# Kernel tuning notes

Measured on AMD Instinct MI355X. Metric: run time of the kernel, lower is better.

The kernel has to match this reference:

```python
import jax, jax.numpy as jnp
import numpy as np

NUM_HEADS = 16
HEAD_DIM = 128  # embed_dim 2048 / 16 heads


def setup_inputs() -> dict:
    key = jax.random.key(0)
    x = jax.random.normal(key, (2, 2048, 2048), dtype=jnp.float32)
    return {"x": x}


def reference(x):
    # EvoAttn forward: V-only causal self-attention (q = k = v = reshaped x).
    B, L, E = x.shape
    H, D = NUM_HEADS, HEAD_DIM
    v = x.reshape(B, L, H, D).transpose(0, 2, 1, 3)  # (B, H, L, D)
    scale = 1.0 / jnp.sqrt(jnp.asarray(D, dtype=x.dtype))
    scores = jnp.einsum("bhqd,bhkd->bhqk", v, v) * scale  # (B, H, L, L)
    causal = jnp.tril(jnp.ones((L, L), dtype=bool))
    scores = jnp.where(causal[None, None], scores, jnp.asarray(-jnp.inf, dtype=scores.dtype))
    p = jax.nn.softmax(scores, axis=-1)
    y = jnp.einsum("bhqk,bhkd->bhqd", p, v)  # (B, H, L, D)
    return y.transpose(0, 2, 1, 3).reshape(B, L, E)
```

## Files before the change

### kernel.cpp

```cpp
#include <hip/hip_runtime.h>


#define TL 2048
#define TE 2048
#define TD 128
#define QB 64
#define KB 64
#define NT 32
#define TILE_B 16384
#define KV_REGION (2 * 16 * NT * TILE_B)
#define WS_NEED (2u * (unsigned)KV_REGION)

typedef __attribute__((ext_vector_type(8))) short bf16x8;
typedef __attribute__((ext_vector_type(4))) float f32x4;
typedef __attribute__((ext_vector_type(8))) unsigned short u16x8;
typedef __attribute__((ext_vector_type(4))) unsigned short u16x4;

#define SCALE_LOG2E 0.12751879f

__device__ __forceinline__ unsigned short f2bf(float f) {
  unsigned int u = __builtin_bit_cast(unsigned int, f);
  u += 0x7fffu + ((u >> 16) & 1u);
  return (unsigned short)(u >> 16);
}

__device__ __forceinline__ f32x4 mfma16(bf16x8 a, bf16x8 b, f32x4 c) {
  return __builtin_amdgcn_mfma_f32_16x16x32_bf16(a, b, c, 0, 0, 0);
}

__device__ __forceinline__ void gl_lds16(const void* g, void* l) {
  __builtin_amdgcn_global_load_lds(
      (__attribute__((address_space(1))) void*)(g),
      (__attribute__((address_space(3))) void*)(l), 16, 0, 0);
}

__device__ __forceinline__ void stage_tile(const float* __restrict__ src,
                                           unsigned short* kv, unsigned short* kvt,
                                           int t) {
  const int kr = (t >> 4) << 2;
  const int d0 = (t & 15) << 3;
  unsigned short c[4][8];
#pragma unroll
  for (int rr = 0; rr < 4; ++rr) {
    const float* p = src + (kr + rr) * TE + d0;
    const float4 a = *(const float4*)p;
    const float4 b = *(const float4*)(p + 4);
    c[rr][0] = f2bf(a.x); c[rr][1] = f2bf(a.y); c[rr][2] = f2bf(a.z); c[rr][3] = f2bf(a.w);
    c[rr][4] = f2bf(b.x); c[rr][5] = f2bf(b.y); c[rr][6] = f2bf(b.z); c[rr][7] = f2bf(b.w);
  }
#pragma unroll
  for (int rr = 0; rr < 4; ++rr) {
    const int r = kr + rr;
    u16x8 o = {c[rr][0], c[rr][1], c[rr][2], c[rr][3],
               c[rr][4], c[rr][5], c[rr][6], c[rr][7]};
    const int off = (r * 256 + d0 * 2) ^ ((r & 7) << 4);
    *(u16x8*)((char*)kv + off) = o;
  }
#pragma unroll
  for (int cc = 0; cc < 8; ++cc) {
    const int d = d0 + cc;
    u16x4 o = {c[0][cc], c[1][cc], c[2][cc], c[3][cc]};
    const int off = (d * 128 + kr * 2) ^ ((d & 7) << 4);
    *(u16x4*)((char*)kvt + off) = o;
  }
}

__device__ __forceinline__ bf16x8 ld256(const unsigned short* base, int row, int inrow) {
  const int off = (row * 256 + inrow) ^ ((row & 7) << 4);
  return *(const bf16x8*)((const char*)base + off);
}
__device__ __forceinline__ bf16x8 ld128(const unsigned short* base, int row, int inrow) {
  const int off = (row * 128 + inrow) ^ ((row & 7) << 4);
  return *(const bf16x8*)((const char*)base + off);
}

__global__ void __launch_bounds__(256)
prepack(const float* __restrict__ x, char* __restrict__ wsb) {
  __shared__ unsigned short kv[QB * TD];
  __shared__ unsigned short kvt[TD * KB];
  const int bid = blockIdx.x;
  const int kt = bid & 31;
  const int bh = bid >> 5;
  const int b = bh >> 4;
  const int h = bh & 15;
  const float* src = x + (size_t)b * TL * TE + h * TD + (size_t)kt * KB * TE;
  stage_tile(src, kv, kvt, threadIdx.x);
  __syncthreads();
  char* gkv = wsb + (size_t)bid * TILE_B;
  char* gkt = wsb + KV_REGION + (size_t)bid * TILE_B;
  const char* lv = (const char*)kv;
  const char* lt = (const char*)kvt;
  const int t = threadIdx.x;
#pragma unroll
  for (int i = 0; i < 4; ++i) {
    *(u16x8*)(gkv + t * 64 + i * 16) = *(const u16x8*)(lv + t * 64 + i * 16);
    *(u16x8*)(gkt + t * 64 + i * 16) = *(const u16x8*)(lt + t * 64 + i * 16);
  }
}

__global__ void __launch_bounds__(256)
evo_attn2(const char* __restrict__ wsb, float* __restrict__ out) {
  __shared__ char smem[3 * TILE_B + 8192];

  const int t = threadIdx.x;
  const int lane = t & 63;
  const int w = t >> 6;
  const int g = lane >> 4;
  const int q15 = lane & 15;

  const int bh = blockIdx.x & 31;
  const int qt = 31 - (blockIdx.x >> 5);
  const int b = bh >> 4;
  const int h = bh & 15;
  const int q0 = qt * QB;

  const char* gkv = wsb + (size_t)bh * (NT * TILE_B);
  const char* gkt = wsb + KV_REGION + (size_t)bh * (NT * TILE_B);

  unsigned short* kvt = (unsigned short*)(smem + 2 * TILE_B);
  unsigned short* plw = (unsigned short*)(smem + 3 * TILE_B) + w * (16 * KB);

#define STAGE_KV(BUFI, KT)                                                 \
  {                                                                        \
    char* dst_ = smem + (BUFI) * TILE_B;                                   \
    const char* src_ = gkv + (KT) * TILE_B;                                \
    _Pragma("unroll")                                                      \
    for (int i_ = 0; i_ < 4; ++i_) {                                       \
      const int c_ = (w * 4 + i_) * 1024;                                  \
      gl_lds16(src_ + c_ + lane * 16, dst_ + c_);                          \
    }                                                                      \
  }
#define STAGE_KT(KT)                                                       \
  {                                                                        \
    char* dst_ = smem + 2 * TILE_B;                                        \
    const char* src_ = gkt + (KT) * TILE_B;                                \
    _Pragma("unroll")                                                      \
    for (int i_ = 0; i_ < 4; ++i_) {                                       \
      const int c_ = (w * 4 + i_) * 1024;                                  \
      gl_lds16(src_ + c_ + lane * 16, dst_ + c_);                          \
    }                                                                      \
  }

  STAGE_KV(0, qt);
  STAGE_KT(qt);
  asm volatile("s_waitcnt vmcnt(0)" ::: "memory");
  __builtin_amdgcn_s_barrier();
  asm volatile("" ::: "memory");

  bf16x8 qf[4];
#pragma unroll
  for (int c = 0; c < 4; ++c)
    qf[c] = ld256((const unsigned short*)smem, 16 * w + q15, c * 64 + g * 16);

  f32x4 acc[8];
#pragma unroll
  for (int dt = 0; dt < 8; ++dt) acc[dt] = (f32x4){0.f, 0.f, 0.f, 0.f};
  float mrun = -1e30f;
  float lrun = 0.f;

  for (int s = 0; s <= qt; ++s) {
    if (s < qt) STAGE_KV((s + 1) & 1, s);

    if (s > 0) {
      if (s < qt) asm volatile("s_waitcnt vmcnt(8)" ::: "memory");
      else        asm volatile("s_waitcnt vmcnt(4)" ::: "memory");
      __builtin_amdgcn_s_barrier();
      asm volatile("" ::: "memory");
    }
    const unsigned short* kv = (const unsigned short*)(smem + (s & 1) * TILE_B);

    float sv[16];
    __builtin_amdgcn_s_setprio(1);
#pragma unroll
    for (int kt2 = 0; kt2 < 4; ++kt2) {
      f32x4 st = (f32x4){0.f, 0.f, 0.f, 0.f};
#pragma unroll
      for (int c = 0; c < 4; ++c) {
        bf16x8 kf = ld256(kv, kt2 * 16 + q15, c * 64 + g * 16);
        st = mfma16(kf, qf[c], st);
      }
#pragma unroll
      for (int r = 0; r < 4; ++r) sv[kt2 * 4 + r] = st[r] * SCALE_LOG2E;
    }
    __builtin_amdgcn_s_setprio(0);

    if (s == 0) {
      const int qrel = 16 * w + q15;
#pragma unroll
      for (int kt2 = 0; kt2 < 4; ++kt2)
#pragma unroll
        for (int r = 0; r < 4; ++r)
          if (kt2 * 16 + g * 4 + r > qrel) sv[kt2 * 4 + r] = -1e30f;
    }

    float tmax = sv[0];
#pragma unroll
    for (int i = 1; i < 16; ++i) tmax = fmaxf(tmax, sv[i]);
    tmax = fmaxf(tmax, __shfl_xor(tmax, 16));
    tmax = fmaxf(tmax, __shfl_xor(tmax, 32));

    const float mnew = fmaxf(mrun, tmax);
    const float al = exp2f(mrun - mnew);
    mrun = mnew;

    float psum = 0.f;
    unsigned short pb[16];
#pragma unroll
    for (int i = 0; i < 16; ++i) {
      const float p = exp2f(sv[i] - mnew);
      psum += p;
      pb[i] = f2bf(p);
    }
    lrun = lrun * al + psum;

#pragma unroll
    for (int kt2 = 0; kt2 < 4; ++kt2) {
      u16x4 o = {pb[kt2 * 4], pb[kt2 * 4 + 1], pb[kt2 * 4 + 2], pb[kt2 * 4 + 3]};
      const int off = (q15 * 128 + kt2 * 32 + g * 8) ^ ((q15 & 7) << 4);
      *(u16x4*)((char*)plw + off) = o;
    }
    asm volatile("s_waitcnt lgkmcnt(0)" ::: "memory");

    if (s > 0) {
      if (s < qt) asm volatile("s_waitcnt vmcnt(4)" ::: "memory");
      else        asm volatile("s_waitcnt vmcnt(0)" ::: "memory");
      __builtin_amdgcn_s_barrier();
      asm volatile("" ::: "memory");
    }

    float ar[4];
#pragma unroll
    for (int r = 0; r < 4; ++r) ar[r] = __shfl(al, g * 4 + r);
#pragma unroll
    for (int dt = 0; dt < 8; ++dt)
#pragma unroll
      for (int r = 0; r < 4; ++r) acc[dt][r] *= ar[r];

    bf16x8 pa0 = ld128(plw, q15, g * 16);
    bf16x8 pa1 = ld128(plw, q15, 64 + g * 16);
    __builtin_amdgcn_s_setprio(1);
#pragma unroll
    for (int dt = 0; dt < 8; ++dt) {
      bf16x8 vb0 = ld128(kvt, dt * 16 + q15, g * 16);
      bf16x8 vb1 = ld128(kvt, dt * 16 + q15, 64 + g * 16);
      acc[dt] = mfma16(pa0, vb0, acc[dt]);
      acc[dt] = mfma16(pa1, vb1, acc[dt]);
    }
    __builtin_amdgcn_s_setprio(0);

    if (s < qt) {
      __builtin_amdgcn_s_barrier();
      asm volatile("" ::: "memory");
      STAGE_KT(s);
    }
  }

  lrun += __shfl_xor(lrun, 16);
  lrun += __shfl_xor(lrun, 32);

  const float inv = 1.f / lrun;
  float ir[4];
#pragma unroll
  for (int r = 0; r < 4; ++r) ir[r] = __shfl(inv, g * 4 + r);

  float* ob = out + ((size_t)b * TL + q0 + 16 * w) * TE + h * TD;
#pragma unroll
  for (int dt = 0; dt < 8; ++dt)
#pragma unroll
    for (int r = 0; r < 4; ++r)
      ob[(g * 4 + r) * TE + dt * 16 + q15] = acc[dt][r] * ir[r];
}

__global__ void __launch_bounds__(256)
evo_attn(const float* __restrict__ x, float* __restrict__ out) {
  __shared__ unsigned short kv[QB * TD];
  __shared__ unsigned short kvt[TD * KB];
  __shared__ unsigned short pl[4 * 16 * KB];

  const int t = threadIdx.x;
  const int lane = t & 63;
  const int w = t >> 6;
  const int g = lane >> 4;
  const int q15 = lane & 15;

  const int bh = blockIdx.x & 31;
  const int qt = 31 - (blockIdx.x >> 5);
  const int b = bh >> 4;
  const int h = bh & 15;
  const float* xb = x + (size_t)b * TL * TE + h * TD;
  const int q0 = qt * QB;

  stage_tile(xb + (size_t)q0 * TE, kv, kvt, t);
  __syncthreads();

  bf16x8 qf[4];
#pragma unroll
  for (int c = 0; c < 4; ++c)
    qf[c] = ld256(kv, 16 * w + q15, c * 64 + g * 16);

  f32x4 acc[8];
#pragma unroll
  for (int dt = 0; dt < 8; ++dt) acc[dt] = (f32x4){0.f, 0.f, 0.f, 0.f};
  float mrun = -1e30f;
  float lrun = 0.f;
  unsigned short* plw = pl + w * (16 * KB);

  for (int s = 0; s <= qt; ++s) {
    if (s > 0) {
      __syncthreads();
      stage_tile(xb + (size_t)(s - 1) * KB * TE, kv, kvt, t);
      __syncthreads();
    }
    float sv[16];
#pragma unroll
    for (int kt2 = 0; kt2 < 4; ++kt2) {
      f32x4 st = (f32x4){0.f, 0.f, 0.f, 0.f};
#pragma unroll
      for (int c = 0; c < 4; ++c) {
        bf16x8 kf = ld256(kv, kt2 * 16 + q15, c * 64 + g * 16);
        st = mfma16(kf, qf[c], st);
      }
#pragma unroll
      for (int r = 0; r < 4; ++r) sv[kt2 * 4 + r] = st[r] * SCALE_LOG2E;
    }
    if (s == 0) {
      const int qrel = 16 * w + q15;
#pragma unroll
      for (int kt2 = 0; kt2 < 4; ++kt2)
#pragma unroll
        for (int r = 0; r < 4; ++r)
          if (kt2 * 16 + g * 4 + r > qrel) sv[kt2 * 4 + r] = -1e30f;
    }
    float tmax = sv[0];
#pragma unroll
    for (int i = 1; i < 16; ++i) tmax = fmaxf(tmax, sv[i]);
    tmax = fmaxf(tmax, __shfl_xor(tmax, 16));
    tmax = fmaxf(tmax, __shfl_xor(tmax, 32));
    const float mnew = fmaxf(mrun, tmax);
    const float al = exp2f(mrun - mnew);
    mrun = mnew;
    float psum = 0.f;
    unsigned short pb[16];
#pragma unroll
    for (int i = 0; i < 16; ++i) {
      const float p = exp2f(sv[i] - mnew);
      psum += p;
      pb[i] = f2bf(p);
    }
    lrun = lrun * al + psum;
#pragma unroll
    for (int kt2 = 0; kt2 < 4; ++kt2) {
      u16x4 o = {pb[kt2 * 4], pb[kt2 * 4 + 1], pb[kt2 * 4 + 2], pb[kt2 * 4 + 3]};
      const int off = (q15 * 128 + kt2 * 32 + g * 8) ^ ((q15 & 7) << 4);
      *(u16x4*)((char*)plw + off) = o;
    }
    asm volatile("s_waitcnt lgkmcnt(0)" ::: "memory");
    float ar[4];
#pragma unroll
    for (int r = 0; r < 4; ++r) ar[r] = __shfl(al, g * 4 + r);
#pragma unroll
    for (int dt = 0; dt < 8; ++dt)
#pragma unroll
      for (int r = 0; r < 4; ++r) acc[dt][r] *= ar[r];
    bf16x8 pa0 = ld128(plw, q15, g * 16);
    bf16x8 pa1 = ld128(plw, q15, 64 + g * 16);
#pragma unroll
    for (int dt = 0; dt < 8; ++dt) {
      bf16x8 vb0 = ld128(kvt, dt * 16 + q15, g * 16);
      bf16x8 vb1 = ld128(kvt, dt * 16 + q15, 64 + g * 16);
      acc[dt] = mfma16(pa0, vb0, acc[dt]);
      acc[dt] = mfma16(pa1, vb1, acc[dt]);
    }
  }

  lrun += __shfl_xor(lrun, 16);
  lrun += __shfl_xor(lrun, 32);
  const float inv = 1.f / lrun;
  float ir[4];
#pragma unroll
  for (int r = 0; r < 4; ++r) ir[r] = __shfl(inv, g * 4 + r);
  float* ob = out + ((size_t)b * TL + q0 + 16 * w) * TE + h * TD;
#pragma unroll
  for (int dt = 0; dt < 8; ++dt)
#pragma unroll
    for (int r = 0; r < 4; ++r)
      ob[(g * 4 + r) * TE + dt * 16 + q15] = acc[dt][r] * ir[r];
}

extern "C" void kernel_launch(void* const* d_in, const int* in_sizes, int n_in,
                              void* d_out, int out_size, void* d_ws, size_t ws_size,
                              hipStream_t stream) {
  const float* x = (const float*)d_in[0];
  float* out = (float*)d_out;
  (void)in_sizes; (void)n_in; (void)out_size;
  if (ws_size >= (size_t)WS_NEED) {
    char* wsb = (char*)d_ws;
    prepack<<<dim3(1024), dim3(256), 0, stream>>>(x, wsb);
    evo_attn2<<<dim3(1024), dim3(256), 0, stream>>>(wsb, out);
  } else {
    evo_attn<<<dim3(1024), dim3(256), 0, stream>>>(x, out);
  }
}
```

Baseline: 99.80 us.

## Use 128-row query tiles with 8 waves sharing K/V staging per block

The main attention kernel now runs 512-thread blocks, each owning 128 query rows split across 8 waves, so every staged K/V tile feeds twice as many queries and global/LDS staging per query halves. Query tiles are issued in an interleaved long/short order to balance the causal workload across CUs. The online softmax folds the scale into an FMA and skips the accumulator rescale when no wave's max grows. The trade-offs are more barriers with idle waves on the diagonal step, a larger LDS footprint, and fewer blocks in flight.

Result: slower. 211.6 us (+112.0%).

```diff
diff --git a/kernel.cpp b/kernel.cpp
--- a/kernel.cpp
+++ b/kernel.cpp
@@ -1,14 +1,14 @@
 #include <hip/hip_runtime.h>
+#include <hip/hip_bf16.h>
 
 
 #define TL 2048
 #define TE 2048
 #define TD 128
-#define QB 64
 #define KB 64
-#define NT 32
+#define NTILES 32
 #define TILE_B 16384
-#define KV_REGION (2 * 16 * NT * TILE_B)
+#define KV_REGION (32 * NTILES * TILE_B)
 #define WS_NEED (2u * (unsigned)KV_REGION)
 
 typedef __attribute__((ext_vector_type(8))) short bf16x8;
@@ -19,9 +19,8 @@
 #define SCALE_LOG2E 0.12751879f
 
 __device__ __forceinline__ unsigned short f2bf(float f) {
-  unsigned int u = __builtin_bit_cast(unsigned int, f);
-  u += 0x7fffu + ((u >> 16) & 1u);
-  return (unsigned short)(u >> 16);
+  __hip_bfloat16 h = __float2bfloat16(f);
+  return __builtin_bit_cast(unsigned short, h);
 }
 
 __device__ __forceinline__ f32x4 mfma16(bf16x8 a, bf16x8 b, f32x4 c) {
@@ -76,7 +75,7 @@
 
 __global__ void __launch_bounds__(256)
 prepack(const float* __restrict__ x, char* __restrict__ wsb) {
-  __shared__ unsigned short kv[QB * TD];
+  __shared__ unsigned short kv[KB * TD];
   __shared__ unsigned short kvt[TD * KB];
   const int bid = blockIdx.x;
   const int kt = bid & 31;
@@ -98,9 +97,9 @@
   }
 }
 
-__global__ void __launch_bounds__(256)
+__global__ void __launch_bounds__(512, 4)
 evo_attn2(const char* __restrict__ wsb, float* __restrict__ out) {
-  __shared__ char smem[3 * TILE_B + 8192];
+  __shared__ char smem[4 * TILE_B];
 
   const int t = threadIdx.x;
   const int lane = t & 63;
@@ -109,48 +108,43 @@
   const int q15 = lane & 15;
 
   const int bh = blockIdx.x & 31;
-  const int qt = 31 - (blockIdx.x >> 5);
+  const int r_ = blockIdx.x >> 5;
+  const int QSEQ[16] = {15, 0, 13, 2, 11, 4, 9, 6, 8, 7, 10, 5, 12, 3, 14, 1};
+  const int q2 = QSEQ[r_];
   const int b = bh >> 4;
   const int h = bh & 15;
-  const int q0 = qt * QB;
-
-  const char* gkv = wsb + (size_t)bh * (NT * TILE_B);
-  const char* gkt = wsb + KV_REGION + (size_t)bh * (NT * TILE_B);
+  const int q0 = q2 * 128;
+  const int nt = 2 * q2 + 2;
+
+  const char* gkv = wsb + (size_t)bh * (NTILES * TILE_B);
+  const char* gkt = wsb + KV_REGION + (size_t)bh * (NTILES * TILE_B);
 
   unsigned short* kvt = (unsigned short*)(smem + 2 * TILE_B);
   unsigned short* plw = (unsigned short*)(smem + 3 * TILE_B) + w * (16 * KB);
 
-#define STAGE_KV(BUFI, KT)                                                 \
+#define STAGE(DSTOFF, SRCBASE, KT)                                         \
   {                                                                        \
-    char* dst_ = smem + (BUFI) * TILE_B;                                   \
-    const char* src_ = gkv + (KT) * TILE_B;                                \
+    char* dst_ = smem + (DSTOFF);                                          \
+    const char* src_ = (SRCBASE) + (size_t)(KT) * TILE_B;                  \
     _Pragma("unroll")                                                      \
-    for (int i_ = 0; i_ < 4; ++i_) {                                       \
-      const int c_ = (w * 4 + i_) * 1024;                                  \
+    for (int i_ = 0; i_ < 2; ++i_) {                                       \
+      const int c_ = (i_ * 8 + w) * 1024;                                  \
       gl_lds16(src_ + c_ + lane * 16, dst_ + c_);                          \
     }                                                                      \
   }
-#define STAGE_KT(KT)                                                       \
-  {                                                                        \
-    char* dst_ = smem + 2 * TILE_B;                                        \
-    const char* src_ = gkt + (KT) * TILE_B;                                \
-    _Pragma("unroll")                                                      \
-    for (int i_ = 0; i_ < 4; ++i_) {                                       \
-      const int c_ = (w * 4 + i_) * 1024;                                  \
-      gl_lds16(src_ + c_ + lane * 16, dst_ + c_);                          \
-    }                                                                      \
-  }
-
-  STAGE_KV(0, qt);
-  STAGE_KT(qt);
+
+  STAGE(0, gkv, 2 * q2);
+  STAGE(TILE_B, gkv, 2 * q2 + 1);
+  STAGE(2 * TILE_B, gkt, 2 * q2);
   asm volatile("s_waitcnt vmcnt(0)" ::: "memory");
   __builtin_amdgcn_s_barrier();
   asm volatile("" ::: "memory");
 
+  const unsigned short* qbuf = (const unsigned short*)(smem + ((w >= 4) ? TILE_B : 0));
   bf16x8 qf[4];
 #pragma unroll
   for (int c = 0; c < 4; ++c)
-    qf[c] = ld256((const unsigned short*)smem, 16 * w + q15, c * 64 + g * 16);
+    qf[c] = ld256(qbuf, (16 * w + q15) & 63, c * 64 + g * 16);
 
   f32x4 acc[8];
 #pragma unroll
@@ -158,101 +152,112 @@
   float mrun = -1e30f;
   float lrun = 0.f;
 
-  for (int s = 0; s <= qt; ++s) {
-    if (s < qt) STAGE_KV((s + 1) & 1, s);
-
+  for (int s = 0; s < nt; ++s) {
     if (s > 0) {
-      if (s < qt) asm volatile("s_waitcnt vmcnt(8)" ::: "memory");
-      else        asm volatile("s_waitcnt vmcnt(4)" ::: "memory");
+      if (s + 1 < nt) asm volatile("s_waitcnt vmcnt(4)" ::: "memory");
+      else            asm volatile("s_waitcnt vmcnt(2)" ::: "memory");
       __builtin_amdgcn_s_barrier();
       asm volatile("" ::: "memory");
     }
     const unsigned short* kv = (const unsigned short*)(smem + (s & 1) * TILE_B);
-
-    float sv[16];
-    __builtin_amdgcn_s_setprio(1);
-#pragma unroll
-    for (int kt2 = 0; kt2 < 4; ++kt2) {
-      f32x4 st = (f32x4){0.f, 0.f, 0.f, 0.f};
-#pragma unroll
-      for (int c = 0; c < 4; ++c) {
-        bf16x8 kf = ld256(kv, kt2 * 16 + q15, c * 64 + g * 16);
-        st = mfma16(kf, qf[c], st);
-      }
-#pragma unroll
-      for (int r = 0; r < 4; ++r) sv[kt2 * 4 + r] = st[r] * SCALE_LOG2E;
-    }
-    __builtin_amdgcn_s_setprio(0);
-
-    if (s == 0) {
-      const int qrel = 16 * w + q15;
-#pragma unroll
-      for (int kt2 = 0; kt2 < 4; ++kt2)
-#pragma unroll
-        for (int r = 0; r < 4; ++r)
-          if (kt2 * 16 + g * 4 + r > qrel) sv[kt2 * 4 + r] = -1e30f;
-    }
-
-    float tmax = sv[0];
-#pragma unroll
-    for (int i = 1; i < 16; ++i) tmax = fmaxf(tmax, sv[i]);
-    tmax = fmaxf(tmax, __shfl_xor(tmax, 16));
-    tmax = fmaxf(tmax, __shfl_xor(tmax, 32));
-
-    const float mnew = fmaxf(mrun, tmax);
-    const float al = exp2f(mrun - mnew);
-    mrun = mnew;
-
-    float psum = 0.f;
-    unsigned short pb[16];
-#pragma unroll
-    for (int i = 0; i < 16; ++i) {
-      const float p = exp2f(sv[i] - mnew);
-      psum += p;
-      pb[i] = f2bf(p);
-    }
-    lrun = lrun * al + psum;
-
-#pragma unroll
-    for (int kt2 = 0; kt2 < 4; ++kt2) {
-      u16x4 o = {pb[kt2 * 4], pb[kt2 * 4 + 1], pb[kt2 * 4 + 2], pb[kt2 * 4 + 3]};
-      const int off = (q15 * 128 + kt2 * 32 + g * 8) ^ ((q15 & 7) << 4);
-      *(u16x4*)((char*)plw + off) = o;
-    }
-    asm volatile("s_waitcnt lgkmcnt(0)" ::: "memory");
+    const bool inactive = (s == 1) && (w < 4);
+
+    float pf[16];
+    if (!inactive) {
+      float sv[16];
+      __builtin_amdgcn_s_setprio(1);
+#pragma unroll
+      for (int kt2 = 0; kt2 < 4; ++kt2) {
+        f32x4 st = (f32x4){0.f, 0.f, 0.f, 0.f};
+#pragma unroll
+        for (int c = 0; c < 4; ++c) {
+          bf16x8 kf = ld256(kv, kt2 * 16 + q15, c * 64 + g * 16);
+          st = mfma16(kf, qf[c], st);
+        }
+#pragma unroll
+        for (int r = 0; r < 4; ++r) sv[kt2 * 4 + r] = st[r];
+      }
+      __builtin_amdgcn_s_setprio(0);
+
+      if (s < 2 && ((s == 0) == (w < 4))) {
+        const int qrel = (16 * w + q15) & 63;
+#pragma unroll
+        for (int kt2 = 0; kt2 < 4; ++kt2)
+#pragma unroll
+          for (int r = 0; r < 4; ++r)
+            if (kt2 * 16 + g * 4 + r > qrel) sv[kt2 * 4 + r] = -1e30f;
+      }
+
+      float m0 = fmaxf(fmaxf(sv[0], sv[1]), fmaxf(sv[2], sv[3]));
+      float m1 = fmaxf(fmaxf(sv[4], sv[5]), fmaxf(sv[6], sv[7]));
+      float m2 = fmaxf(fmaxf(sv[8], sv[9]), fmaxf(sv[10], sv[11]));
+      float m3 = fmaxf(fmaxf(sv[12], sv[13]), fmaxf(sv[14], sv[15]));
+      float tmax = fmaxf(fmaxf(m0, m1), fmaxf(m2, m3));
+      tmax = fmaxf(tmax, __shfl_xor(tmax, 16));
+      tmax = fmaxf(tmax, __shfl_xor(tmax, 32));
+
+      if (__all(tmax <= mrun)) {
+        const float nmc = -mrun * SCALE_LOG2E;
+#pragma unroll
+        for (int i = 0; i < 16; ++i) pf[i] = exp2f(fmaf(sv[i], SCALE_LOG2E, nmc));
+      } else {
+        const float mnew = fmaxf(mrun, tmax);
+        const float al = exp2f((mrun - mnew) * SCALE_LOG2E);
+        mrun = mnew;
+        const float nmc = -mnew * SCALE_LOG2E;
+#pragma unroll
+        for (int i = 0; i < 16; ++i) pf[i] = exp2f(fmaf(sv[i], SCALE_LOG2E, nmc));
+        lrun *= al;
+        float ar[4];
+#pragma unroll
+        for (int r = 0; r < 4; ++r) ar[r] = __shfl(al, g * 4 + r);
+#pragma unroll
+        for (int dt = 0; dt < 8; ++dt)
+#pragma unroll
+          for (int r = 0; r < 4; ++r) acc[dt][r] *= ar[r];
+      }
+
+      float s01 = (pf[0] + pf[1]) + (pf[2] + pf[3]);
+      float s23 = (pf[4] + pf[5]) + (pf[6] + pf[7]);
+      float s45 = (pf[8] + pf[9]) + (pf[10] + pf[11]);
+      float s67 = (pf[12] + pf[13]) + (pf[14] + pf[15]);
+      lrun += (s01 + s23) + (s45 + s67);
+
+#pragma unroll
+      for (int kt2 = 0; kt2 < 4; ++kt2) {
+        u16x4 o = {f2bf(pf[kt2 * 4]), f2bf(pf[kt2 * 4 + 1]),
+                   f2bf(pf[kt2 * 4 + 2]), f2bf(pf[kt2 * 4 + 3])};
+        const int off = (q15 * 128 + kt2 * 32 + g * 8) ^ ((q15 & 7) << 4);
+        *(u16x4*)((char*)plw + off) = o;
+      }
+      asm volatile("s_waitcnt lgkmcnt(0)" ::: "memory");
+    }
 
     if (s > 0) {
-      if (s < qt) asm volatile("s_waitcnt vmcnt(4)" ::: "memory");
-      else        asm volatile("s_waitcnt vmcnt(0)" ::: "memory");
+      if (s + 1 < nt) asm volatile("s_waitcnt vmcnt(2)" ::: "memory");
+      else            asm volatile("s_waitcnt vmcnt(0)" ::: "memory");
       __builtin_amdgcn_s_barrier();
       asm volatile("" ::: "memory");
     }
 
-    float ar[4];
-#pragma unroll
-    for (int r = 0; r < 4; ++r) ar[r] = __shfl(al, g * 4 + r);
-#pragma unroll
-    for (int dt = 0; dt < 8; ++dt)
-#pragma unroll
-      for (int r = 0; r < 4; ++r) acc[dt][r] *= ar[r];
-
-    bf16x8 pa0 = ld128(plw, q15, g * 16);
-    bf16x8 pa1 = ld128(plw, q15, 64 + g * 16);
-    __builtin_amdgcn_s_setprio(1);
-#pragma unroll
-    for (int dt = 0; dt < 8; ++dt) {
-      bf16x8 vb0 = ld128(kvt, dt * 16 + q15, g * 16);
-      bf16x8 vb1 = ld128(kvt, dt * 16 + q15, 64 + g * 16);
-      acc[dt] = mfma16(pa0, vb0, acc[dt]);
-      acc[dt] = mfma16(pa1, vb1, acc[dt]);
-    }
-    __builtin_amdgcn_s_setprio(0);
-
-    if (s < qt) {
-      __builtin_amdgcn_s_barrier();
-      asm volatile("" ::: "memory");
-      STAGE_KT(s);
-    }
+    if (!inactive) {
+      bf16x8 pa0 = ld128(plw, q15, g * 16);
+      bf16x8 pa1 = ld128(plw, q15, 64 + g * 16);
+      __builtin_amdgcn_s_setprio(1);
+#pragma unroll
+      for (int dt = 0; dt < 8; ++dt) {
+        bf16x8 vb0 = ld128(kvt, dt * 16 + q15, g * 16);
+        bf16x8 vb1 = ld128(kvt, dt * 16 + q15, 64 + g * 16);
+        acc[dt] = mfma16(pa0, vb0, acc[dt]);
+        acc[dt] = mfma16(pa1, vb1, acc[dt]);
+      }
+      __builtin_amdgcn_s_setprio(0);
+    }
+
+    __builtin_amdgcn_s_barrier();
+    asm volatile("" ::: "memory");
+    if (s + 1 < nt) STAGE(2 * TILE_B, gkt, (s == 0) ? (2 * q2 + 1) : (s - 1));
+    if (s + 2 < nt) STAGE((s & 1) * TILE_B, gkv, s);
   }
 
   lrun += __shfl_xor(lrun, 16);
@@ -273,7 +278,7 @@
 
 __global__ void __launch_bounds__(256)
 evo_attn(const float* __restrict__ x, float* __restrict__ out) {
-  __shared__ unsigned short kv[QB * TD];
+  __shared__ unsigned short kv[KB * TD];
   __shared__ unsigned short kvt[TD * KB];
   __shared__ unsigned short pl[4 * 16 * KB];
 
@@ -288,7 +293,7 @@
   const int b = bh >> 4;
   const int h = bh & 15;
   const float* xb = x + (size_t)b * TL * TE + h * TD;
-  const int q0 = qt * QB;
+  const int q0 = qt * KB;
 
   stage_tile(xb + (size_t)q0 * TE, kv, kvt, t);
   __syncthreads();
@@ -396,7 +401,7 @@
   if (ws_size >= (size_t)WS_NEED) {
     char* wsb = (char*)d_ws;
     prepack<<<dim3(1024), dim3(256), 0, stream>>>(x, wsb);
-    evo_attn2<<<dim3(1024), dim3(256), 0, stream>>>(wsb, out);
+    evo_attn2<<<dim3(512), dim3(512), 0, stream>>>(wsb, out);
   } else {
     evo_attn<<<dim3(1024), dim3(256), 0, stream>>>(x, out);
   }
```
